# Kernel tuning notes

Hardware: AMD Instinct MI355X
Metric: run time of the kernel (lower is better)

The kernel has to match this reference:

```python
import jax, jax.numpy as jnp
import numpy as np


def _conv3x3(x, w, b):
    # standard 3x3 conv, stride 1, padding 1, NCHW/OIHW
    y = jax.lax.conv_general_dilated(
        x, w, window_strides=(1, 1), padding=((1, 1), (1, 1)),
        dimension_numbers=('NCHW', 'OIHW', 'NCHW'))
    return y + b[None, :, None, None]


def _deform_conv3x3(x, offset, w, b):
    # torchvision-style DeformConv2d: kernel 3x3, stride 1, pad 1, dilation 1,
    # 1 offset group, no mask. offset: [B, 18, H, W] with (dy, dx) per tap.
    B, C, H, W = x.shape
    K = 9
    off = offset.reshape(B, K, 2, H, W)
    ky = (jnp.arange(K) // 3 - 1).astype(x.dtype)[None, :, None, None]
    kx = (jnp.arange(K) % 3 - 1).astype(x.dtype)[None, :, None, None]
    # fractional sample positions per output pixel and kernel tap: [B, K, H, W]
    sy = off[:, :, 0] + ky + jnp.arange(H, dtype=x.dtype)[None, None, :, None]
    sx = off[:, :, 1] + kx + jnp.arange(W, dtype=x.dtype)[None, None, None, :]
    y0f = jnp.floor(sy)
    x0f = jnp.floor(sx)
    dy = sy - y0f
    dx = sx - x0f
    y0 = y0f.astype(jnp.int32)
    x0 = x0f.astype(jnp.int32)

    def sample_b(xb, yi, xi):
        # xb: [C,H,W], yi/xi: [K,H,W] -> [C,K,H,W], zero outside bounds
        valid = (yi >= 0) & (yi < H) & (xi >= 0) & (xi < W)
        yc = jnp.clip(yi, 0, H - 1)
        xc = jnp.clip(xi, 0, W - 1)
        return xb[:, yc, xc] * valid[None].astype(xb.dtype)

    def bilinear_b(xb, y0b, x0b, dyb, dxb):
        v00 = sample_b(xb, y0b, x0b)
        v01 = sample_b(xb, y0b, x0b + 1)
        v10 = sample_b(xb, y0b + 1, x0b)
        v11 = sample_b(xb, y0b + 1, x0b + 1)
        w00 = ((1 - dyb) * (1 - dxb))[None]
        w01 = ((1 - dyb) * dxb)[None]
        w10 = (dyb * (1 - dxb))[None]
        w11 = (dyb * dxb)[None]
        return v00 * w00 + v01 * w01 + v10 * w10 + v11 * w11

    samp = jax.vmap(bilinear_b)(x, y0, x0, dy, dx)  # [B, C, K, H, W]
    Co, Ci = w.shape[0], w.shape[1]
    out = jnp.einsum('oik,bikhw->bohw', w.reshape(Co, Ci, K), samp)
    return out + b[None, :, None, None]


def setup_inputs() -> dict:
    key = jax.random.key(0)
    ks = jax.random.split(key, 5)
    B, C, H, W = 4, 128, 96, 96
    lr = jax.random.normal(ks[0], (B, C, H, W), jnp.float32)
    hr = jax.random.normal(ks[1], (B, C, H, W), jnp.float32)
    w_off = jax.random.normal(ks[2], (18, 2 * C, 3, 3), jnp.float32) * 0.02
    b_off = jnp.zeros((18,), jnp.float32)
    w_def = jax.random.normal(ks[3], (C, C, 3, 3), jnp.float32) / np.float32(np.sqrt(C * 9))
    b_def = jax.random.normal(ks[4], (C,), jnp.float32) * 0.01
    return {"lr_features": lr, "hr_features": hr, "w_off": w_off,
            "b_off": b_off, "w_def": w_def, "b_def": b_def}


def reference(lr_features, hr_features, w_off, b_off, w_def, b_def):
    inp = jnp.concatenate([lr_features, hr_features], axis=1)  # [B, 2C, H, W]
    offset = _conv3x3(inp, w_off, b_off)                        # [B, 18, H, W]
    return _deform_conv3x3(hr_features, offset, w_def, b_def)   # [B, C, H, W]
```

## Files before the change

kernel.cpp:

```cpp
#include <hip/hip_runtime.h>
#include <hip/hip_bf16.h>

#define HH 96
#define WW 96
#define CC 128
#define C2 256
#define PLANE (HH*WW)
#define NGRP 6
#define GP 8
#define NG 16
#define KSG 72
#define ROWS 13
#define NPCHK (ROWS*WW)
#define PCHK_PAD 1280
#define HPX 48

typedef __attribute__((ext_vector_type(8))) short bf16x8;
typedef __attribute__((ext_vector_type(4))) float f32x4;
typedef __attribute__((ext_vector_type(4))) unsigned int u32x4;

__device__ __forceinline__ int swz(int row, int byte_in_row) {
    return row * 128 + (byte_in_row ^ ((row & 7) << 4));
}

__device__ __forceinline__ void gload_lds16(const void* g, void* l) {
    __builtin_amdgcn_global_load_lds(
        (const __attribute__((address_space(1))) char*)g,
        (__attribute__((address_space(3))) char*)l, 16, 0, 0);
}

__device__ __forceinline__ unsigned pack2(float a, float b) {
    return (unsigned)__bfloat16_as_ushort(__float2bfloat16(a)) |
           ((unsigned)__bfloat16_as_ushort(__float2bfloat16(b)) << 16);
}

#define MFMA16(A,B,C) __builtin_amdgcn_mfma_f32_16x16x32_bf16((A),(B),(C),0,0,0)

#define VMW4() { asm volatile("s_waitcnt vmcnt(4)" ::: "memory"); __builtin_amdgcn_sched_barrier(0); }
#define VMW0() { asm volatile("s_waitcnt vmcnt(0)" ::: "memory"); __builtin_amdgcn_sched_barrier(0); }
#define LGKM0_BAR() { asm volatile("s_waitcnt lgkmcnt(0)" ::: "memory"); \
    __builtin_amdgcn_sched_barrier(0); __builtin_amdgcn_s_barrier(); \
    __builtin_amdgcn_sched_barrier(0); }
#define RAW_BAR() { __builtin_amdgcn_sched_barrier(0); __builtin_amdgcn_s_barrier(); \
    __builtin_amdgcn_sched_barrier(0); }

__global__ __launch_bounds__(256) void prep_kernel(
    const float* __restrict__ hr, const float* __restrict__ lr,
    const float* __restrict__ w_def, const float* __restrict__ w_off,
    unsigned short* __restrict__ hrbf, unsigned short* __restrict__ lrbf,
    unsigned short* __restrict__ wpad, unsigned short* __restrict__ wop)
{
    const int bid = blockIdx.x;
    const int tid = threadIdx.x;
    if (bid < 4608) {
        const bool is_hr = bid < 2304;
        const float* src0 = is_hr ? hr : lr;
        unsigned short* o = is_hr ? hrbf : lrbf;
        int idx = (is_hr ? bid : bid - 2304) * 256 + tid;
        int hw = idx % PLANE;
        int t  = idx / PLANE;
        int g  = t & 15;
        int b  = t >> 4;
        const float* src = src0 + ((size_t)(b * CC + g * GP)) * PLANE + hw;
        unsigned pk[4];
#pragma unroll
        for (int j = 0; j < 4; ++j)
            pk[j] = pack2(src[(size_t)(2*j) * PLANE], src[(size_t)(2*j+1) * PLANE]);
        u32x4 v = {pk[0], pk[1], pk[2], pk[3]};
        *reinterpret_cast<u32x4*>(o + (size_t)idx * 8) = v;
    } else if (bid < 5184) {
        int i = (bid - 4608) * 256 + tid;
        int oc = i / (NG * KSG);
        int r  = i - oc * (NG * KSG);
        int g  = r / KSG;
        int s  = r - g * KSG;
        int tap = s >> 3;
        int icoff = s & 7;
        wpad[i] = __bfloat16_as_ushort(__float2bfloat16(
            w_def[(size_t)(oc * CC + g * GP + icoff) * 9 + tap]));
    } else {
        int i = (bid - 5184) * 256 + tid;
        int oc = i / (32 * KSG);
        int r  = i - oc * (32 * KSG);
        int g  = r / KSG;
        int s  = r - g * KSG;
        int tap = s >> 3;
        int icoff = s & 7;
        int c = g * 8 + icoff;
        float v = (oc < 18) ? w_off[(size_t)(oc * C2 + c) * 9 + tap] : 0.f;
        wop[i] = __bfloat16_as_ushort(__float2bfloat16(v));
    }
}

__global__ __launch_bounds__(256) void wcvt_kernel(const float* __restrict__ w,
                                                   unsigned short* __restrict__ o)
{
    int i = blockIdx.x * 256 + threadIdx.x;
    if (i < CC * NG * KSG) {
        int oc = i / (NG * KSG);
        int r  = i - oc * (NG * KSG);
        int g  = r / KSG;
        int s  = r - g * KSG;
        int tap = s >> 3;
        int icoff = s & 7;
        o[i] = __bfloat16_as_ushort(__float2bfloat16(
            w[(size_t)(oc * CC + g * GP + icoff) * 9 + tap]));
    }
}

__global__ __launch_bounds__(256) void cvt8_kernel(const float* __restrict__ src0,
                                                   unsigned short* __restrict__ o)
{
    int idx = blockIdx.x * 256 + threadIdx.x;
    int hw = idx % PLANE;
    int t  = idx / PLANE;
    int g  = t & 15;
    int b  = t >> 4;
    const float* src = src0 + ((size_t)(b * CC + g * GP)) * PLANE + hw;
    unsigned pk[4];
#pragma unroll
    for (int j = 0; j < 4; ++j)
        pk[j] = pack2(src[(size_t)(2*j) * PLANE], src[(size_t)(2*j+1) * PLANE]);
    u32x4 v = {pk[0], pk[1], pk[2], pk[3]};
    *reinterpret_cast<u32x4*>(o + (size_t)idx * 8) = v;
}

__global__ __launch_bounds__(256) void offset_conv_kernel(
    const float* __restrict__ lr, const float* __restrict__ hr,
    const float* __restrict__ w_off, float* __restrict__ outp)
{
    __shared__ float tile[2][324];
    const int bid = blockIdx.x;
    const int q   = bid % NGRP;
    const int t   = bid / NGRP;
    const int b   = t / 36;
    const int rr  = t % 36;
    const int h0  = (rr / 6) * 16;
    const int w0  = (rr % 6) * 16;
    const int tid = threadIdx.x;
    const int py  = tid >> 4;
    const int px  = tid & 15;

    const int c0 = (C2 * q) / NGRP, c1 = (C2 * (q + 1)) / NGRP;
    const float* srcp = (q < 3) ? lr : hr;
    const int cofs = (q < 3) ? 0 : CC;

    int gy0 = h0 - 1 + tid / 18, gx0 = w0 - 1 + tid % 18;
    bool ok0 = (unsigned)gy0 < (unsigned)HH && (unsigned)gx0 < (unsigned)WW;
    int off0 = gy0 * WW + gx0;
    int j1 = tid + 256;
    int gy1 = h0 - 1 + j1 / 18, gx1 = w0 - 1 + j1 % 18;
    bool ok1 = (j1 < 324) && (unsigned)gy1 < (unsigned)HH && (unsigned)gx1 < (unsigned)WW;
    int off1 = gy1 * WW + gx1;

    float acc[18];
#pragma unroll
    for (int oc = 0; oc < 18; ++oc) acc[oc] = 0.f;

    const float* pl = srcp + (size_t)(b * CC + c0 - cofs) * PLANE;
    float p0 = ok0 ? pl[off0] : 0.f;
    float p1 = ok1 ? pl[off1] : 0.f;

    for (int c = c0; c < c1; ++c) {
        float* tb = tile[c & 1];
        tb[tid] = p0;
        if (j1 < 324) tb[j1] = p1;
        __syncthreads();
        if (c + 1 < c1) {
            const float* pn = srcp + (size_t)(b * CC + c + 1 - cofs) * PLANE;
            p0 = ok0 ? pn[off0] : 0.f;
            p1 = ok1 ? pn[off1] : 0.f;
        }
        float tv[9];
#pragma unroll
        for (int ky = 0; ky < 3; ++ky)
#pragma unroll
            for (int kx = 0; kx < 3; ++kx)
                tv[ky*3+kx] = tb[(py+ky)*18 + px + kx];
#pragma unroll
        for (int oc = 0; oc < 18; ++oc) {
            const float* wp = w_off + (size_t)(oc * C2 + c) * 9;
#pragma unroll
            for (int tap = 0; tap < 9; ++tap)
                acc[oc] = fmaf(wp[tap], tv[tap], acc[oc]);
        }
    }
#pragma unroll
    for (int oc = 0; oc < 18; ++oc)
        outp[((size_t)(b*CC + q*18 + oc)) * PLANE + (h0+py)*WW + (w0+px)] = acc[oc];
}

__global__ __launch_bounds__(768, 6) void offset_mfma_kernel(
    const unsigned short* __restrict__ lrbf, const unsigned short* __restrict__ hrbf,
    const unsigned short* __restrict__ wop, const float* __restrict__ b_off,
    float* __restrict__ offw)
{
    __shared__ __align__(16) unsigned short planes[2][2][3*WW*8];
    __shared__ __align__(16) unsigned short wgt0[2][32*64];
    __shared__ __align__(16) unsigned short wgt1[2][32*8];
    __shared__ __align__(16) unsigned short samp0[2][WW*64];
    __shared__ __align__(16) unsigned short samp1[2][WW*8];

    const int rawb = blockIdx.x;
    const int bid  = (rawb & 7) * 48 + (rawb >> 3);
    const int b    = bid / HH;
    const int h    = bid % HH;
    const int tid  = threadIdx.x;

    const int pri = tid / 96, ppx = tid - (tid / 96) * 96;
    const int prow = min(max(h - 1 + pri, 0), HH - 1);

    const int woc = tid / 9, wsl = tid % 9;
    float4 wv0, wv1;

#define ISSUE_P2(PAIR, PB) { \
    if (tid < 288) { \
        int gA_ = 2*(PAIR), gB_ = gA_ + 1; \
        const unsigned short* bA_ = (gA_ < 16 ? lrbf : hrbf); \
        const unsigned short* bB_ = (gB_ < 16 ? lrbf : hrbf); \
        gload_lds16(bA_ + ((size_t)(b*16 + (gA_ & 15)) * PLANE + prow*WW + ppx) * 8, \
                    (char*)planes[PB][0] + tid*16); \
        gload_lds16(bB_ + ((size_t)(b*16 + (gB_ & 15)) * PLANE + prow*WW + ppx) * 8, \
                    (char*)planes[PB][1] + tid*16); \
    } }
#define ISSUE_W2(PAIR) { \
    if (tid < 288) { \
        wv0 = *reinterpret_cast<const float4*>(wop + ((size_t)(woc*32 + 2*(PAIR)    ))*KSG + wsl*8); \
        wv1 = *reinterpret_cast<const float4*>(wop + ((size_t)(woc*32 + 2*(PAIR) + 1))*KSG + wsl*8); \
    } }
#define WRITE_W2() { \
    if (tid < 288) { \
        if (wsl < 8) { \
            *reinterpret_cast<float4*>((char*)wgt0[0] + swz(woc, wsl*16)) = wv0; \
            *reinterpret_cast<float4*>((char*)wgt0[1] + swz(woc, wsl*16)) = wv1; \
        } else { \
            *reinterpret_cast<float4*>((char*)wgt1[0] + woc*16) = wv0; \
            *reinterpret_cast<float4*>((char*)wgt1[1] + woc*16) = wv1; \
        } \
    } }

    const int tap1 = tid / WW, px1 = tid - (tid / WW) * WW;
    const int ky1 = tap1 / 3 - 1, kx1 = tap1 % 3 - 1;
    const int row1 = h + ky1, x1 = px1 + kx1;
    const bool ok1 = (unsigned)row1 < (unsigned)HH && (unsigned)x1 < (unsigned)WW;
    const int ro1 = ((ky1+1)*WW + x1) * 16;
    const int wr1 = px1*128 + ((tap1*16) ^ ((px1 & 7) << 4));
    const int x2 = tid + 1;
    const bool ok2 = (tid < 96) && (h + 1 < HH) && (x2 < WW);
    const int ro2 = (2*WW + x2) * 16;
    const int wr2 = tid * 16;

    const int lane = tid & 63;
    const int wid  = tid >> 6;
    const int ocg  = wid / 6;
    const int pxg  = wid - ocg * 6;
    const int l15  = lane & 15;
    const int l4   = lane >> 4;
    const int rowA = ocg*16 + l15;
    const int rowB = pxg*16 + l15;
    const bf16x8 zf = {};

    f32x4 acc = (f32x4){0.f, 0.f, 0.f, 0.f};

#define MFMA_O2() { \
    _Pragma("unroll") \
    for (int q_ = 0; q_ < 2; ++q_) { \
        bf16x8 a0_ = *reinterpret_cast<const bf16x8*>((char*)wgt0[q_] + swz(rowA, l4*16)); \
        bf16x8 a1_ = *reinterpret_cast<const bf16x8*>((char*)wgt0[q_] + swz(rowA, 64 + l4*16)); \
        bf16x8 a2_ = *reinterpret_cast<const bf16x8*>((char*)wgt1[q_] + rowA*16); \
        if (l4) a2_ = zf; \
        bf16x8 b0_ = *reinterpret_cast<const bf16x8*>((char*)samp0[q_] + swz(rowB, l4*16)); \
        bf16x8 b1_ = *reinterpret_cast<const bf16x8*>((char*)samp0[q_] + swz(rowB, 64 + l4*16)); \
        bf16x8 b2_ = *reinterpret_cast<const bf16x8*>((char*)samp1[q_] + rowB*16); \
        acc = MFMA16(a0_, b0_, acc); \
        acc = MFMA16(a1_, b1_, acc); \
        acc = MFMA16(a2_, b2_, acc); \
    } }

    ISSUE_W2(0);
    ISSUE_P2(0, 0);
    __syncthreads();

    for (int p2 = 0; p2 < 16; ++p2) {
        const int sb = p2 & 1;
        WRITE_W2();
        if (p2 < 15) {
            ISSUE_W2(p2 + 1);
            ISSUE_P2(p2 + 1, sb ^ 1);
            VMW4();
        } else {
            VMW0();
        }
        RAW_BAR();
        {
            u32x4 vA = {0u, 0u, 0u, 0u}, vB = {0u, 0u, 0u, 0u};
            if (ok1) {
                vA = *reinterpret_cast<const u32x4*>((const char*)planes[sb][0] + ro1);
                vB = *reinterpret_cast<const u32x4*>((const char*)planes[sb][1] + ro1);
            }
            *reinterpret_cast<u32x4*>((char*)samp0[0] + wr1) = vA;
            *reinterpret_cast<u32x4*>((char*)samp0[1] + wr1) = vB;
            if (tid < 96) {
                u32x4 wA = {0u, 0u, 0u, 0u}, wB = {0u, 0u, 0u, 0u};
                if (ok2) {
                    wA = *reinterpret_cast<const u32x4*>((const char*)planes[sb][0] + ro2);
                    wB = *reinterpret_cast<const u32x4*>((const char*)planes[sb][1] + ro2);
                }
                *reinterpret_cast<u32x4*>((char*)samp1[0] + wr2) = wA;
                *reinterpret_cast<u32x4*>((char*)samp1[1] + wr2) = wB;
            }
        }
        LGKM0_BAR();
        __builtin_amdgcn_s_setprio(1);
        MFMA_O2();
        __builtin_amdgcn_s_setprio(0);
        RAW_BAR();
    }

#pragma unroll
    for (int r = 0; r < 4; ++r) {
        int oc = ocg*16 + l4*4 + r;
        if (oc < 18)
            offw[((size_t)(b*18 + oc)) * PLANE + h*WW + pxg*16 + l15] = acc[r] + b_off[oc];
    }
#undef ISSUE_P2
#undef ISSUE_W2
#undef WRITE_W2
#undef MFMA_O2
}

__global__ __launch_bounds__(384, 6) void deform3_kernel(
    const unsigned short* __restrict__ hrbf, const unsigned short* __restrict__ wpad,
    const float* __restrict__ b_def, const float* __restrict__ offw,
    float* __restrict__ outp)
{
    __shared__ __align__(16) unsigned short wgt0[CC*64];
    __shared__ __align__(16) unsigned short wgt1[CC*8];
    __shared__ __align__(16) unsigned short samp0[HPX*64];
    __shared__ __align__(16) unsigned short samp1[HPX*8];
    __shared__ __align__(16) float4 gw4[9*HPX];
    __shared__ __align__(8)  short4 gyo[9*HPX];
    __shared__ float bias_lds[CC];

    const int rawb = blockIdx.x;
    const int bid  = (rawb & 7) * 96 + (rawb >> 3);
    const int b    = bid / 192;
    const int t2   = bid % 192;
    const int h    = t2 >> 1;
    const int half = t2 & 1;
    const int px0  = half * HPX;
    const int tid  = threadIdx.x;

    float4 wv0, wv1, wv2;
    const int c0 = tid,        w0oc = c0 / 9, w0s = c0 % 9;
    const int c1 = tid + 384,  w1oc = c1 / 9, w1s = c1 % 9;
    const int c2 = tid + 768,  w2oc = c2 / 9, w2s = c2 % 9;

#define ISSUE_WGT(G) { \
    wv0 = *reinterpret_cast<const float4*>(wpad + ((size_t)(w0oc*NG + (G))*KSG + w0s*8)); \
    wv1 = *reinterpret_cast<const float4*>(wpad + ((size_t)(w1oc*NG + (G))*KSG + w1s*8)); \
    wv2 = *reinterpret_cast<const float4*>(wpad + ((size_t)(w2oc*NG + (G))*KSG + w2s*8)); }
#define WRITE_WGT() { \
    if (w0s < 8) *reinterpret_cast<float4*>((char*)wgt0 + swz(w0oc, w0s*16)) = wv0; \
    else         *reinterpret_cast<float4*>((char*)wgt1 + w0oc*16) = wv0; \
    if (w1s < 8) *reinterpret_cast<float4*>((char*)wgt0 + swz(w1oc, w1s*16)) = wv1; \
    else         *reinterpret_cast<float4*>((char*)wgt1 + w1oc*16) = wv1; \
    if (w2s < 8) *reinterpret_cast<float4*>((char*)wgt0 + swz(w2oc, w2s*16)) = wv2; \
    else         *reinterpret_cast<float4*>((char*)wgt1 + w2oc*16) = wv2; }

    ISSUE_WGT(0);

    for (int it = tid; it < 9 * HPX; it += 384) {
        int tap = it / HPX;
        int px  = it - tap * HPX;
        int gx  = px0 + px;
        int hw  = h * WW + gx;
        float offy = offw[((size_t)(b*18 + 2*tap    )) * PLANE + hw];
        float offx = offw[((size_t)(b*18 + 2*tap + 1)) * PLANE + hw];
        float sy = (float)h  + (float)(tap/3 - 1) + offy;
        float sx = (float)gx + (float)(tap%3 - 1) + offx;
        float y0f = floorf(sy), x0f = floorf(sx);
        float dy = sy - y0f, dx = sx - x0f;
        int y0 = (int)y0f, x0 = (int)x0f;
        bool y0v = (unsigned)y0       < (unsigned)HH;
        bool y1v = (unsigned)(y0 + 1) < (unsigned)HH;
        bool x0v = (unsigned)x0       < (unsigned)WW;
        bool x1v = (unsigned)(x0 + 1) < (unsigned)WW;
        float ody = 1.f - dy, odx = 1.f - dx;
        float4 wv;
        wv.x = (y0v && x0v) ? ody*odx : 0.f;
        wv.y = (y0v && x1v) ? ody*dx  : 0.f;
        wv.z = (y1v && x0v) ? dy*odx  : 0.f;
        wv.w = (y1v && x1v) ? dy*dx   : 0.f;
        short4 o4;
        o4.x = (short)min(max(y0,     0), HH-1);
        o4.y = (short)min(max(y0 + 1, 0), HH-1);
        o4.z = (short)min(max(x0,     0), WW-1);
        o4.w = (short)min(max(x0 + 1, 0), WW-1);
        gw4[it] = wv;
        gyo[it] = o4;
    }
    if (tid < CC) bias_lds[tid] = b_def[tid];
    __syncthreads();

    const int lane = tid & 63;
    const int wid  = tid >> 6;
    const int ocg  = wid / 3;
    const int pxg  = wid - ocg * 3;
    const int l15  = lane & 15;
    const int l4   = lane >> 4;

    f32x4 acc[4];
#pragma unroll
    for (int mf = 0; mf < 4; ++mf) acc[mf] = (f32x4){0.f, 0.f, 0.f, 0.f};

    const int rowB = pxg*16 + l15;
    const bf16x8 zf = {};

#define MFMA_G() { \
    _Pragma("unroll") \
    for (int ks = 0; ks < 2; ++ks) { \
        int kb = ks*64 + l4*16; \
        bf16x8 bb = *reinterpret_cast<const bf16x8*>((char*)samp0 + swz(rowB, kb)); \
        _Pragma("unroll") \
        for (int mf = 0; mf < 4; ++mf) { \
            bf16x8 aa = *reinterpret_cast<const bf16x8*>((char*)wgt0 + swz(ocg*64 + mf*16 + l15, kb)); \
            acc[mf] = MFMA16(aa, bb, acc[mf]); \
        } \
    } \
    { \
        bf16x8 bb = *reinterpret_cast<const bf16x8*>((char*)samp1 + rowB*16); \
        _Pragma("unroll") \
        for (int mf = 0; mf < 4; ++mf) { \
            bf16x8 aa = *reinterpret_cast<const bf16x8*>((char*)wgt1 + (ocg*64 + mf*16 + l15)*16); \
            if (l4) aa = zf; \
            acc[mf] = MFMA16(aa, bb, acc[mf]); \
        } \
    } }

    const unsigned short* gb = hrbf + (size_t)(b * NG) * PLANE * 8;

    for (int g = 0; g < NG; ++g) {
        WRITE_WGT();
        if (g < NG - 1) ISSUE_WGT(g + 1);
        const unsigned short* gpl = gb + (size_t)g * PLANE * 8;
        for (int it = tid; it < 9 * HPX; it += 384) {
            float4 w4 = gw4[it];
            short4 o4 = gyo[it];
            int ra = (int)o4.x * WW, rb = (int)o4.y * WW;
            u32x4 q00 = *reinterpret_cast<const u32x4*>(gpl + (size_t)(ra + o4.z) * 8);
            u32x4 q01 = *reinterpret_cast<const u32x4*>(gpl + (size_t)(ra + o4.w) * 8);
            u32x4 q10 = *reinterpret_cast<const u32x4*>(gpl + (size_t)(rb + o4.z) * 8);
            u32x4 q11 = *reinterpret_cast<const u32x4*>(gpl + (size_t)(rb + o4.w) * 8);
            float sv[GP];
#pragma unroll
            for (int j = 0; j < 4; ++j) {
                float a00 = __uint_as_float(q00[j] << 16), b00 = __uint_as_float(q00[j] & 0xffff0000u);
                float a01 = __uint_as_float(q01[j] << 16), b01 = __uint_as_float(q01[j] & 0xffff0000u);
                float a10 = __uint_as_float(q10[j] << 16), b10 = __uint_as_float(q10[j] & 0xffff0000u);
                float a11 = __uint_as_float(q11[j] << 16), b11 = __uint_as_float(q11[j] & 0xffff0000u);
                sv[2*j]   = fmaf(w4.x, a00, fmaf(w4.y, a01, fmaf(w4.z, a10, w4.w*a11)));
                sv[2*j+1] = fmaf(w4.x, b00, fmaf(w4.y, b01, fmaf(w4.z, b10, w4.w*b11)));
            }
            unsigned pk0 = pack2(sv[0], sv[1]), pk1 = pack2(sv[2], sv[3]);
            unsigned pk2 = pack2(sv[4], sv[5]), pk3 = pack2(sv[6], sv[7]);
            u32x4 pv = {pk0, pk1, pk2, pk3};
            int tap = it / HPX;
            int px  = it - tap * HPX;
            if (tap < 8)
                *reinterpret_cast<u32x4*>((char*)samp0 + swz(px, tap*16)) = pv;
            else
                *reinterpret_cast<u32x4*>((char*)samp1 + px*16) = pv;
        }
        LGKM0_BAR();
        __builtin_amdgcn_s_setprio(1);
        MFMA_G();
        __builtin_amdgcn_s_setprio(0);
        RAW_BAR();
    }

#pragma unroll
    for (int mf = 0; mf < 4; ++mf)
#pragma unroll
        for (int r = 0; r < 4; ++r) {
            int oc = ocg*64 + mf*16 + l4*4 + r;
            float bd = bias_lds[oc];
            outp[((size_t)(b*CC + oc)) * PLANE + h*WW + px0 + pxg*16 + l15] = acc[mf][r] + bd;
        }
#undef ISSUE_WGT
#undef WRITE_WGT
#undef MFMA_G
}

template<bool HRBF, bool OFFWS>
__global__ __launch_bounds__(768, 6) void deform2_kernel(
    const float* __restrict__ hr, const unsigned short* __restrict__ hrbf,
    const float* __restrict__ b_off, const unsigned short* __restrict__ wpad,
    const float* __restrict__ b_def, const float* __restrict__ offw,
    float* __restrict__ outp)
{
    __shared__ __align__(16) unsigned short planes[2][PCHK_PAD*8];
    __shared__ __align__(16) unsigned short wgt0[CC*64];
    __shared__ __align__(16) unsigned short wgt1[CC*8];
    __shared__ __align__(16) unsigned short samp0[WW*64];
    __shared__ __align__(16) unsigned short samp1[WW*8];
    __shared__ __align__(8)  float2 geom[9*97];
    __shared__ float bias_lds[CC];

    const int rawb = blockIdx.x;
    const int bid  = (rawb & 7) * 48 + (rawb >> 3);
    const int b    = bid / HH;
    const int h    = bid % HH;
    const int tid  = threadIdx.x;
    const int r0   = min(max(h - 6, 0), HH - ROWS);

    const float* hrb = hr + (size_t)b * CC * PLANE;

    float4 wv0, wv1;
    const int wc0oc = tid / 9, wc0s = tid % 9;
    const int wt2   = (tid < 384) ? tid + 768 : tid;
    const int wc1oc = wt2 / 9, wc1s = wt2 % 9;
    const int pc2   = (tid < 512) ? tid + 768 : tid;
    const int pcs   = min(pc2, NPCHK - 1);

#define ISSUE_WGT(G) { \
    wv0 = *reinterpret_cast<const float4*>(wpad + ((size_t)(wc0oc*NG + (G))*KSG + wc0s*8)); \
    wv1 = *reinterpret_cast<const float4*>(wpad + ((size_t)(wc1oc*NG + (G))*KSG + wc1s*8)); }
#define WRITE_WGT() { \
    if (wc0s < 8) *reinterpret_cast<float4*>((char*)wgt0 + swz(wc0oc, wc0s*16)) = wv0; \
    else          *reinterpret_cast<float4*>((char*)wgt1 + wc0oc*16) = wv0; \
    if (tid < 384) { \
        if (wc1s < 8) *reinterpret_cast<float4*>((char*)wgt0 + swz(wc1oc, wc1s*16)) = wv1; \
        else          *reinterpret_cast<float4*>((char*)wgt1 + wc1oc*16) = wv1; \
    } }

#define ISSUE_PLANES(G, PB) { \
    const unsigned short* src_ = hrbf + ((size_t)(b*NG + (G))*PLANE + r0*WW)*8; \
    gload_lds16(src_ + (size_t)tid*8, (char*)planes[PB] + tid*16); \
    gload_lds16(src_ + (size_t)pcs*8, (char*)planes[PB] + pc2*16); }

#define STAGE_DIRECT(G, PB) { \
    for (int p = tid; p < NPCHK; p += 768) { \
        int r_ = p / WW, x_ = p - (p / WW) * WW; \
        const float* s_ = hrb + (size_t)((G)*GP) * PLANE + (r0 + r_)*WW + x_; \
        unsigned pk_[4]; \
        _Pragma("unroll") \
        for (int j = 0; j < 4; ++j) \
            pk_[j] = pack2(s_[(size_t)(2*j)*PLANE], s_[(size_t)(2*j+1)*PLANE]); \
        u32x4 v_ = {pk_[0], pk_[1], pk_[2], pk_[3]}; \
        *reinterpret_cast<u32x4*>((char*)planes[PB] + p*16) = v_; \
    } }

    if (HRBF) ISSUE_PLANES(0, 0);
    ISSUE_WGT(0);

    for (int t = tid; t < 9 * WW; t += 768) {
        int tap = t / WW;
        int px  = t - tap * WW;
        int hw  = h * WW + px;
        float offy, offx;
        if (OFFWS) {
            offy = offw[((size_t)(b*18 + 2*tap    )) * PLANE + hw];
            offx = offw[((size_t)(b*18 + 2*tap + 1)) * PLANE + hw];
        } else {
            offy = b_off[2*tap]; offx = b_off[2*tap + 1];
#pragma unroll
            for (int q = 0; q < NGRP; ++q) {
                offy += outp[((size_t)(b*CC + q*18 + 2*tap    )) * PLANE + hw];
                offx += outp[((size_t)(b*CC + q*18 + 2*tap + 1)) * PLANE + hw];
            }
        }
        geom[tap*97 + px] = make_float2((float)h  + (float)(tap/3 - 1) + offy,
                                        (float)px + (float)(tap%3 - 1) + offx);
    }
    if (tid < CC) bias_lds[tid] = b_def[tid];
    if (!HRBF) STAGE_DIRECT(0, 0);
    __syncthreads();

    const int lane = tid & 63;
    const int wid  = tid >> 6;
    const int ocg4 = wid / 3;
    const int pxg  = wid - ocg4 * 3;
    const int l15  = lane & 15;
    const int l4   = lane >> 4;

    f32x4 acc[2][2];
#pragma unroll
    for (int mf = 0; mf < 2; ++mf)
#pragma unroll
        for (int nf = 0; nf < 2; ++nf)
            acc[mf][nf] = (f32x4){0.f, 0.f, 0.f, 0.f};

    const int rowA0 = ocg4*32 + l15, rowA1 = rowA0 + 16;
    const int rowB0 = pxg*32 + l15,  rowB1 = rowB0 + 16;
    const bf16x8 zf = {};

#define MFMA_G() { \
    bf16x8 a00_ = *reinterpret_cast<const bf16x8*>((char*)wgt0 + swz(rowA0, l4*16)); \
    bf16x8 a10_ = *reinterpret_cast<const bf16x8*>((char*)wgt0 + swz(rowA1, l4*16)); \
    bf16x8 a01_ = *reinterpret_cast<const bf16x8*>((char*)wgt0 + swz(rowA0, 64 + l4*16)); \
    bf16x8 a11_ = *reinterpret_cast<const bf16x8*>((char*)wgt0 + swz(rowA1, 64 + l4*16)); \
    bf16x8 a02_ = *reinterpret_cast<const bf16x8*>((char*)wgt1 + rowA0*16); \
    bf16x8 a12_ = *reinterpret_cast<const bf16x8*>((char*)wgt1 + rowA1*16); \
    if (l4) { a02_ = zf; a12_ = zf; } \
    const char* s0_ = (const char*)samp0; \
    const char* s1_ = (const char*)samp1; \
    bf16x8 b00_ = *reinterpret_cast<const bf16x8*>(s0_ + swz(rowB0, l4*16)); \
    bf16x8 b10_ = *reinterpret_cast<const bf16x8*>(s0_ + swz(rowB1, l4*16)); \
    bf16x8 b01_ = *reinterpret_cast<const bf16x8*>(s0_ + swz(rowB0, 64 + l4*16)); \
    bf16x8 b11_ = *reinterpret_cast<const bf16x8*>(s0_ + swz(rowB1, 64 + l4*16)); \
    bf16x8 b02_ = *reinterpret_cast<const bf16x8*>(s1_ + rowB0*16); \
    bf16x8 b12_ = *reinterpret_cast<const bf16x8*>(s1_ + rowB1*16); \
    acc[0][0] = MFMA16(a00_, b00_, acc[0][0]); \
    acc[0][1] = MFMA16(a00_, b10_, acc[0][1]); \
    acc[1][0] = MFMA16(a10_, b00_, acc[1][0]); \
    acc[1][1] = MFMA16(a10_, b10_, acc[1][1]); \
    acc[0][0] = MFMA16(a01_, b01_, acc[0][0]); \
    acc[0][1] = MFMA16(a01_, b11_, acc[0][1]); \
    acc[1][0] = MFMA16(a11_, b01_, acc[1][0]); \
    acc[1][1] = MFMA16(a11_, b11_, acc[1][1]); \
    acc[0][0] = MFMA16(a02_, b02_, acc[0][0]); \
    acc[0][1] = MFMA16(a02_, b12_, acc[0][1]); \
    acc[1][0] = MFMA16(a12_, b02_, acc[1][0]); \
    acc[1][1] = MFMA16(a12_, b12_, acc[1][1]); }

    for (int g = 0; g < NG; ++g) {
        const int pb = g & 1;
        WRITE_WGT();
        if (g < NG - 1) {
            ISSUE_WGT(g + 1);
            if (HRBF) { ISSUE_PLANES(g + 1, pb ^ 1); }
            else      { STAGE_DIRECT(g + 1, pb ^ 1); }
            if (HRBF) { VMW4(); }
        } else {
            if (HRBF) { VMW0(); }
        }
        for (int it = tid; it < 9 * WW; it += 768) {
            int tap = it / WW;
            int px  = it - tap * WW;
            float2 s2 = geom[tap*97 + px];
            float sy = s2.x, sx = s2.y;
            float y0f = floorf(sy), x0f = floorf(sx);
            float dy = sy - y0f, dx = sx - x0f;
            int y0 = (int)y0f, x0 = (int)x0f;
            bool y0v = (unsigned)y0       < (unsigned)HH;
            bool y1v = (unsigned)(y0 + 1) < (unsigned)HH;
            bool x0v = (unsigned)x0       < (unsigned)WW;
            bool x1v = (unsigned)(x0 + 1) < (unsigned)WW;
            float ody = 1.f - dy, odx = 1.f - dx;
            float w00 = (y0v && x0v) ? ody*odx : 0.f;
            float w01 = (y0v && x1v) ? ody*dx  : 0.f;
            float w10 = (y1v && x0v) ? dy*odx  : 0.f;
            float w11 = (y1v && x1v) ? dy*dx   : 0.f;
            int y0c = min(max(y0, 0), HH-1), y1c = min(max(y0+1, 0), HH-1);
            int x0c = min(max(x0, 0), WW-1), x1c = min(max(x0+1, 0), WW-1);
            float sv[GP];
            bool ng = (y0v && (unsigned)(y0 - r0) >= (unsigned)ROWS) ||
                      (y1v && (unsigned)(y1c - r0) >= (unsigned)ROWS);
            if (__builtin_expect(!ng, 1)) {
                int ra = min(max(y0c - r0, 0), ROWS-1);
                int rb = min(max(y1c - r0, 0), ROWS-1);
                const char* pbase = (const char*)planes[pb];
                u32x4 q00 = *reinterpret_cast<const u32x4*>(pbase + (ra*WW + x0c)*16);
                u32x4 q01 = *reinterpret_cast<const u32x4*>(pbase + (ra*WW + x1c)*16);
                u32x4 q10 = *reinterpret_cast<const u32x4*>(pbase + (rb*WW + x0c)*16);
                u32x4 q11 = *reinterpret_cast<const u32x4*>(pbase + (rb*WW + x1c)*16);
#pragma unroll
                for (int j = 0; j < 4; ++j) {
                    float a00 = __uint_as_float(q00[j] << 16), b00 = __uint_as_float(q00[j] & 0xffff0000u);
                    float a01 = __uint_as_float(q01[j] << 16), b01 = __uint_as_float(q01[j] & 0xffff0000u);
                    float a10 = __uint_as_float(q10[j] << 16), b10 = __uint_as_float(q10[j] & 0xffff0000u);
                    float a11 = __uint_as_float(q11[j] << 16), b11 = __uint_as_float(q11[j] & 0xffff0000u);
                    sv[2*j]   = fmaf(w00, a00, fmaf(w01, a01, fmaf(w10, a10, w11*a11)));
                    sv[2*j+1] = fmaf(w00, b00, fmaf(w01, b01, fmaf(w10, b10, w11*b11)));
                }
            } else {
                const float* base = hrb + (size_t)(g*GP) * PLANE;
#pragma unroll
                for (int j = 0; j < GP; ++j) {
                    const float* p = base + (size_t)j * PLANE;
                    sv[j] = fmaf(w00, p[y0c*WW + x0c], fmaf(w01, p[y0c*WW + x1c],
                            fmaf(w10, p[y1c*WW + x0c], w11 * p[y1c*WW + x1c])));
                }
            }
            unsigned pk0 = pack2(sv[0], sv[1]), pk1 = pack2(sv[2], sv[3]);
            unsigned pk2 = pack2(sv[4], sv[5]), pk3 = pack2(sv[6], sv[7]);
            u32x4 pv = {pk0, pk1, pk2, pk3};
            if (tap < 8)
                *reinterpret_cast<u32x4*>((char*)samp0 + swz(px, tap*16)) = pv;
            else
                *reinterpret_cast<u32x4*>((char*)samp1 + px*16) = pv;
        }
        LGKM0_BAR();
        __builtin_amdgcn_s_setprio(1);
        MFMA_G();
        __builtin_amdgcn_s_setprio(0);
        RAW_BAR();
    }

#pragma unroll
    for (int mf = 0; mf < 2; ++mf)
#pragma unroll
        for (int r = 0; r < 4; ++r) {
            int oc = ocg4*32 + mf*16 + l4*4 + r;
            float bd = bias_lds[oc];
#pragma unroll
            for (int nf = 0; nf < 2; ++nf) {
                int px = pxg*32 + nf*16 + l15;
                outp[((size_t)(b*CC + oc)) * PLANE + h*WW + px] = acc[mf][nf][r] + bd;
            }
        }
#undef ISSUE_WGT
#undef WRITE_WGT
#undef ISSUE_PLANES
#undef STAGE_DIRECT
#undef MFMA_G
}

extern "C" void kernel_launch(void* const* d_in, const int* in_sizes, int n_in,
                              void* d_out, int out_size, void* d_ws, size_t ws_size,
                              hipStream_t stream)
{
    const float* lr    = (const float*)d_in[0];
    const float* hr    = (const float*)d_in[1];
    const float* w_off = (const float*)d_in[2];
    const float* b_off = (const float*)d_in[3];
    const float* w_def = (const float*)d_in[4];
    const float* b_def = (const float*)d_in[5];
    float* outp = (float*)d_out;

    const size_t wpad_b = (size_t)CC * NG * KSG * 2 + 256;
    const size_t hrbf_b = (size_t)4 * NG * PLANE * GP * 2;
    const size_t lrbf_b = hrbf_b;
    const size_t woff_b = (size_t)32 * 32 * KSG * 2 + 256;
    const size_t offw_b = (size_t)4 * 18 * PLANE * 4;

    unsigned short* wpad = (unsigned short*)d_ws;
    unsigned short* hrbf = (unsigned short*)((char*)d_ws + wpad_b);
    unsigned short* lrbf = (unsigned short*)((char*)d_ws + wpad_b + hrbf_b);
    unsigned short* wop  = (unsigned short*)((char*)d_ws + wpad_b + hrbf_b + lrbf_b);
    float*          offw = (float*)((char*)d_ws + wpad_b + hrbf_b + lrbf_b + woff_b);

    const bool full     = ws_size >= wpad_b + hrbf_b + lrbf_b + woff_b + offw_b;
    const bool use_hrbf = ws_size >= wpad_b + hrbf_b + lrbf_b;

    if (full) {
        prep_kernel<<<5472, 256, 0, stream>>>(hr, lr, w_def, w_off,
                                              hrbf, lrbf, wpad, wop);
        offset_mfma_kernel<<<4*HH, 768, 0, stream>>>(lrbf, hrbf, wop, b_off, offw);
        deform3_kernel<<<4*HH*2, 384, 0, stream>>>(hrbf, wpad, b_def, offw, outp);
    } else {
        wcvt_kernel<<<(CC*NG*KSG + 255)/256, 256, 0, stream>>>(w_def, wpad);
        if (use_hrbf)
            cvt8_kernel<<<(4*NG*PLANE)/256, 256, 0, stream>>>(hr, hrbf);
        offset_conv_kernel<<<4*36*NGRP, 256, 0, stream>>>(lr, hr, w_off, outp);
        if (use_hrbf)
            deform2_kernel<true, false><<<4*HH, 768, 0, stream>>>(
                hr, hrbf, b_off, wpad, b_def, offw, outp);
        else
            deform2_kernel<false, false><<<4*HH, 768, 0, stream>>>(
                hr, hrbf, b_off, wpad, b_def, offw, outp);
    }
}
```

Before: 84.83 us.

## Double-buffer weights and samples in deform3 kernel, keep tap geometry in registers

The deform3 kernel now double-buffers the weight and sampled-input LDS tiles, so the next channel group's bilinear sampling and weight store overlap the current group's MFMAs. This leaves one barrier per group instead of two. Per-thread tap geometry (bilinear weights and byte offsets) is computed once and kept in registers, which removes the gw4/gyo LDS tables and their reloads every group. The cost is twice the LDS for the buffers and more registers, and launch bounds drop from 6 to 5 waves-per-EU to allow for that.

```diff
diff --git a/kernel.cpp b/kernel.cpp
--- a/kernel.cpp
+++ b/kernel.cpp
@@ -329,17 +329,15 @@
 #undef MFMA_O2
 }
 
-__global__ __launch_bounds__(384, 6) void deform3_kernel(
+__global__ __launch_bounds__(384, 5) void deform3_kernel(
     const unsigned short* __restrict__ hrbf, const unsigned short* __restrict__ wpad,
     const float* __restrict__ b_def, const float* __restrict__ offw,
     float* __restrict__ outp)
 {
-    __shared__ __align__(16) unsigned short wgt0[CC*64];
-    __shared__ __align__(16) unsigned short wgt1[CC*8];
-    __shared__ __align__(16) unsigned short samp0[HPX*64];
-    __shared__ __align__(16) unsigned short samp1[HPX*8];
-    __shared__ __align__(16) float4 gw4[9*HPX];
-    __shared__ __align__(8)  short4 gyo[9*HPX];
+    __shared__ __align__(16) unsigned short wgt0[2][CC*64];
+    __shared__ __align__(16) unsigned short wgt1[2][CC*8];
+    __shared__ __align__(16) unsigned short samp0[2][HPX*64];
+    __shared__ __align__(16) unsigned short samp1[2][HPX*8];
     __shared__ float bias_lds[CC];
 
     const int rawb = blockIdx.x;
@@ -360,19 +358,19 @@
     wv0 = *reinterpret_cast<const float4*>(wpad + ((size_t)(w0oc*NG + (G))*KSG + w0s*8)); \
     wv1 = *reinterpret_cast<const float4*>(wpad + ((size_t)(w1oc*NG + (G))*KSG + w1s*8)); \
     wv2 = *reinterpret_cast<const float4*>(wpad + ((size_t)(w2oc*NG + (G))*KSG + w2s*8)); }
-#define WRITE_WGT() { \
-    if (w0s < 8) *reinterpret_cast<float4*>((char*)wgt0 + swz(w0oc, w0s*16)) = wv0; \
-    else         *reinterpret_cast<float4*>((char*)wgt1 + w0oc*16) = wv0; \
-    if (w1s < 8) *reinterpret_cast<float4*>((char*)wgt0 + swz(w1oc, w1s*16)) = wv1; \
-    else         *reinterpret_cast<float4*>((char*)wgt1 + w1oc*16) = wv1; \
-    if (w2s < 8) *reinterpret_cast<float4*>((char*)wgt0 + swz(w2oc, w2s*16)) = wv2; \
-    else         *reinterpret_cast<float4*>((char*)wgt1 + w2oc*16) = wv2; }
+#define WRITE_WGT(SB) { \
+    if (w0s < 8) *reinterpret_cast<float4*>((char*)wgt0[SB] + swz(w0oc, w0s*16)) = wv0; \
+    else         *reinterpret_cast<float4*>((char*)wgt1[SB] + w0oc*16) = wv0; \
+    if (w1s < 8) *reinterpret_cast<float4*>((char*)wgt0[SB] + swz(w1oc, w1s*16)) = wv1; \
+    else         *reinterpret_cast<float4*>((char*)wgt1[SB] + w1oc*16) = wv1; \
+    if (w2s < 8) *reinterpret_cast<float4*>((char*)wgt0[SB] + swz(w2oc, w2s*16)) = wv2; \
+    else         *reinterpret_cast<float4*>((char*)wgt1[SB] + w2oc*16) = wv2; }
 
     ISSUE_WGT(0);
 
-    for (int it = tid; it < 9 * HPX; it += 384) {
-        int tap = it / HPX;
-        int px  = it - tap * HPX;
+    float4 w1_; int o1a, o1b, o1c, o1d, wr1;
+    {
+        int tap = tid / HPX, px = tid - (tid / HPX) * HPX;
         int gx  = px0 + px;
         int hw  = h * WW + gx;
         float offy = offw[((size_t)(b*18 + 2*tap    )) * PLANE + hw];
@@ -382,26 +380,86 @@
         float y0f = floorf(sy), x0f = floorf(sx);
         float dy = sy - y0f, dx = sx - x0f;
         int y0 = (int)y0f, x0 = (int)x0f;
-        bool y0v = (unsigned)y0       < (unsigned)HH;
-        bool y1v = (unsigned)(y0 + 1) < (unsigned)HH;
-        bool x0v = (unsigned)x0       < (unsigned)WW;
-        bool x1v = (unsigned)(x0 + 1) < (unsigned)WW;
+        bool y0v = (unsigned)y0 < (unsigned)HH, y1v = (unsigned)(y0+1) < (unsigned)HH;
+        bool x0v = (unsigned)x0 < (unsigned)WW, x1v = (unsigned)(x0+1) < (unsigned)WW;
         float ody = 1.f - dy, odx = 1.f - dx;
-        float4 wv;
-        wv.x = (y0v && x0v) ? ody*odx : 0.f;
-        wv.y = (y0v && x1v) ? ody*dx  : 0.f;
-        wv.z = (y1v && x0v) ? dy*odx  : 0.f;
-        wv.w = (y1v && x1v) ? dy*dx   : 0.f;
-        short4 o4;
-        o4.x = (short)min(max(y0,     0), HH-1);
-        o4.y = (short)min(max(y0 + 1, 0), HH-1);
-        o4.z = (short)min(max(x0,     0), WW-1);
-        o4.w = (short)min(max(x0 + 1, 0), WW-1);
-        gw4[it] = wv;
-        gyo[it] = o4;
+        w1_.x = (y0v && x0v) ? ody*odx : 0.f;
+        w1_.y = (y0v && x1v) ? ody*dx  : 0.f;
+        w1_.z = (y1v && x0v) ? dy*odx  : 0.f;
+        w1_.w = (y1v && x1v) ? dy*dx   : 0.f;
+        int ra = min(max(y0,0),HH-1)*WW,  rb = min(max(y0+1,0),HH-1)*WW;
+        int xa = min(max(x0,0),WW-1),     xb = min(max(x0+1,0),WW-1);
+        o1a = (ra+xa)*16; o1b = (ra+xb)*16; o1c = (rb+xa)*16; o1d = (rb+xb)*16;
+        wr1 = px*128 + ((tap*16) ^ ((px & 7) << 4));
+    }
+    const bool has2 = tid < HPX;
+    float4 w2_; int o2a=0, o2b=0, o2c=0, o2d=0, wr2=0;
+    if (has2) {
+        int gx = px0 + tid;
+        int hw = h * WW + gx;
+        float offy = offw[((size_t)(b*18 + 16)) * PLANE + hw];
+        float offx = offw[((size_t)(b*18 + 17)) * PLANE + hw];
+        float sy = (float)h  + 1.f + offy;
+        float sx = (float)gx + 1.f + offx;
+        float y0f = floorf(sy), x0f = floorf(sx);
+        float dy = sy - y0f, dx = sx - x0f;
+        int y0 = (int)y0f, x0 = (int)x0f;
+        bool y0v = (unsigned)y0 < (unsigned)HH, y1v = (unsigned)(y0+1) < (unsigned)HH;
+        bool x0v = (unsigned)x0 < (unsigned)WW, x1v = (unsigned)(x0+1) < (unsigned)WW;
+        float ody = 1.f - dy, odx = 1.f - dx;
+        w2_.x = (y0v && x0v) ? ody*odx : 0.f;
+        w2_.y = (y0v && x1v) ? ody*dx  : 0.f;
+        w2_.z = (y1v && x0v) ? dy*odx  : 0.f;
+        w2_.w = (y1v && x1v) ? dy*dx   : 0.f;
+        int ra = min(max(y0,0),HH-1)*WW,  rb = min(max(y0+1,0),HH-1)*WW;
+        int xa = min(max(x0,0),WW-1),     xb = min(max(x0+1,0),WW-1);
+        o2a = (ra+xa)*16; o2b = (ra+xb)*16; o2c = (rb+xa)*16; o2d = (rb+xb)*16;
+        wr2 = tid * 16;
     }
     if (tid < CC) bias_lds[tid] = b_def[tid];
-    __syncthreads();
+
+    const unsigned short* gb = hrbf + (size_t)(b * NG) * PLANE * 8;
+
+#define BUILD_G(G, SB) { \
+    const char* gpl_ = (const char*)(gb + (size_t)(G) * PLANE * 8); \
+    { \
+        u32x4 q00 = *reinterpret_cast<const u32x4*>(gpl_ + o1a); \
+        u32x4 q01 = *reinterpret_cast<const u32x4*>(gpl_ + o1b); \
+        u32x4 q10 = *reinterpret_cast<const u32x4*>(gpl_ + o1c); \
+        u32x4 q11 = *reinterpret_cast<const u32x4*>(gpl_ + o1d); \
+        float sv[8]; \
+        _Pragma("unroll") \
+        for (int j = 0; j < 4; ++j) { \
+            float a00 = __uint_as_float(q00[j] << 16), b00 = __uint_as_float(q00[j] & 0xffff0000u); \
+            float a01 = __uint_as_float(q01[j] << 16), b01 = __uint_as_float(q01[j] & 0xffff0000u); \
+            float a10 = __uint_as_float(q10[j] << 16), b10 = __uint_as_float(q10[j] & 0xffff0000u); \
+            float a11 = __uint_as_float(q11[j] << 16), b11 = __uint_as_float(q11[j] & 0xffff0000u); \
+            sv[2*j]   = fmaf(w1_.x, a00, fmaf(w1_.y, a01, fmaf(w1_.z, a10, w1_.w*a11))); \
+            sv[2*j+1] = fmaf(w1_.x, b00, fmaf(w1_.y, b01, fmaf(w1_.z, b10, w1_.w*b11))); \
+        } \
+        u32x4 pv = {pack2(sv[0],sv[1]), pack2(sv[2],sv[3]), \
+                    pack2(sv[4],sv[5]), pack2(sv[6],sv[7])}; \
+        *reinterpret_cast<u32x4*>((char*)samp0[SB] + wr1) = pv; \
+    } \
+    if (has2) { \
+        u32x4 q00 = *reinterpret_cast<const u32x4*>(gpl_ + o2a); \
+        u32x4 q01 = *reinterpret_cast<const u32x4*>(gpl_ + o2b); \
+        u32x4 q10 = *reinterpret_cast<const u32x4*>(gpl_ + o2c); \
+        u32x4 q11 = *reinterpret_cast<const u32x4*>(gpl_ + o2d); \
+        float sv[8]; \
+        _Pragma("unroll") \
+        for (int j = 0; j < 4; ++j) { \
+            float a00 = __uint_as_float(q00[j] << 16), b00 = __uint_as_float(q00[j] & 0xffff0000u); \
+            float a01 = __uint_as_float(q01[j] << 16), b01 = __uint_as_float(q01[j] & 0xffff0000u); \
+            float a10 = __uint_as_float(q10[j] << 16), b10 = __uint_as_float(q10[j] & 0xffff0000u); \
+            float a11 = __uint_as_float(q11[j] << 16), b11 = __uint_as_float(q11[j] & 0xffff0000u); \
+            sv[2*j]   = fmaf(w2_.x, a00, fmaf(w2_.y, a01, fmaf(w2_.z, a10, w2_.w*a11))); \
+            sv[2*j+1] = fmaf(w2_.x, b00, fmaf(w2_.y, b01, fmaf(w2_.z, b10, w2_.w*b11))); \
+        } \
+        u32x4 pv = {pack2(sv[0],sv[1]), pack2(sv[2],sv[3]), \
+                    pack2(sv[4],sv[5]), pack2(sv[6],sv[7])}; \
+        *reinterpret_cast<u32x4*>((char*)samp1[SB] + wr2) = pv; \
+    } }
 
     const int lane = tid & 63;
     const int wid  = tid >> 6;
@@ -417,66 +475,43 @@
     const int rowB = pxg*16 + l15;
     const bf16x8 zf = {};
 
-#define MFMA_G() { \
+#define MFMA_G(SB) { \
     _Pragma("unroll") \
     for (int ks = 0; ks < 2; ++ks) { \
         int kb = ks*64 + l4*16; \
-        bf16x8 bb = *reinterpret_cast<const bf16x8*>((char*)samp0 + swz(rowB, kb)); \
+        bf16x8 bb = *reinterpret_cast<const bf16x8*>((char*)samp0[SB] + swz(rowB, kb)); \
         _Pragma("unroll") \
         for (int mf = 0; mf < 4; ++mf) { \
-            bf16x8 aa = *reinterpret_cast<const bf16x8*>((char*)wgt0 + swz(ocg*64 + mf*16 + l15, kb)); \
+            bf16x8 aa = *reinterpret_cast<const bf16x8*>((char*)wgt0[SB] + swz(ocg*64 + mf*16 + l15, kb)); \
             acc[mf] = MFMA16(aa, bb, acc[mf]); \
         } \
     } \
     { \
-        bf16x8 bb = *reinterpret_cast<const bf16x8*>((char*)samp1 + rowB*16); \
+        bf16x8 bb = *reinterpret_cast<const bf16x8*>((char*)samp1[SB] + rowB*16); \
         _Pragma("unroll") \
         for (int mf = 0; mf < 4; ++mf) { \
-            bf16x8 aa = *reinterpret_cast<const bf16x8*>((char*)wgt1 + (ocg*64 + mf*16 + l15)*16); \
+            bf16x8 aa = *reinterpret_cast<const bf16x8*>((char*)wgt1[SB] + (ocg*64 + mf*16 + l15)*16); \
             if (l4) aa = zf; \
             acc[mf] = MFMA16(aa, bb, acc[mf]); \
         } \
     } }
 
-    const unsigned short* gb = hrbf + (size_t)(b * NG) * PLANE * 8;
+    WRITE_WGT(0);
+    ISSUE_WGT(1);
+    BUILD_G(0, 0);
+    LGKM0_BAR();
 
     for (int g = 0; g < NG; ++g) {
-        WRITE_WGT();
-        if (g < NG - 1) ISSUE_WGT(g + 1);
-        const unsigned short* gpl = gb + (size_t)g * PLANE * 8;
-        for (int it = tid; it < 9 * HPX; it += 384) {
-            float4 w4 = gw4[it];
-            short4 o4 = gyo[it];
-            int ra = (int)o4.x * WW, rb = (int)o4.y * WW;
-            u32x4 q00 = *reinterpret_cast<const u32x4*>(gpl + (size_t)(ra + o4.z) * 8);
-            u32x4 q01 = *reinterpret_cast<const u32x4*>(gpl + (size_t)(ra + o4.w) * 8);
-            u32x4 q10 = *reinterpret_cast<const u32x4*>(gpl + (size_t)(rb + o4.z) * 8);
-            u32x4 q11 = *reinterpret_cast<const u32x4*>(gpl + (size_t)(rb + o4.w) * 8);
-            float sv[GP];
-#pragma unroll
-            for (int j = 0; j < 4; ++j) {
-                float a00 = __uint_as_float(q00[j] << 16), b00 = __uint_as_float(q00[j] & 0xffff0000u);
-                float a01 = __uint_as_float(q01[j] << 16), b01 = __uint_as_float(q01[j] & 0xffff0000u);
-                float a10 = __uint_as_float(q10[j] << 16), b10 = __uint_as_float(q10[j] & 0xffff0000u);
-                float a11 = __uint_as_float(q11[j] << 16), b11 = __uint_as_float(q11[j] & 0xffff0000u);
-                sv[2*j]   = fmaf(w4.x, a00, fmaf(w4.y, a01, fmaf(w4.z, a10, w4.w*a11)));
-                sv[2*j+1] = fmaf(w4.x, b00, fmaf(w4.y, b01, fmaf(w4.z, b10, w4.w*b11)));
-            }
-            unsigned pk0 = pack2(sv[0], sv[1]), pk1 = pack2(sv[2], sv[3]);
-            unsigned pk2 = pack2(sv[4], sv[5]), pk3 = pack2(sv[6], sv[7]);
-            u32x4 pv = {pk0, pk1, pk2, pk3};
-            int tap = it / HPX;
-            int px  = it - tap * HPX;
-            if (tap < 8)
-                *reinterpret_cast<u32x4*>((char*)samp0 + swz(px, tap*16)) = pv;
-            else
-                *reinterpret_cast<u32x4*>((char*)samp1 + px*16) = pv;
-        }
+        const int cur = g & 1;
+        if (g + 1 < NG) {
+            WRITE_WGT(cur ^ 1);
+            if (g + 2 < NG) ISSUE_WGT(g + 2);
+            BUILD_G(g + 1, cur ^ 1);
+        }
+        __builtin_amdgcn_s_setprio(1);
+        MFMA_G(cur);
+        __builtin_amdgcn_s_setprio(0);
         LGKM0_BAR();
-        __builtin_amdgcn_s_setprio(1);
-        MFMA_G();
-        __builtin_amdgcn_s_setprio(0);
-        RAW_BAR();
     }
 
 #pragma unroll
@@ -489,6 +524,7 @@
         }
 #undef ISSUE_WGT
 #undef WRITE_WGT
+#undef BUILD_G
 #undef MFMA_G
 }
 
```

Result: slower. 141.3 us (+66.6%).
